# Kernel optimization log

Hardware: AMD Instinct MI355X
Metric: run time of the kernel (lower is better)

Reference implementation:

```python
import jax, jax.numpy as jnp
import numpy as np

INTERVAL = 0.02

def setup_inputs() -> dict:
    key = jax.random.key(0)
    ks = jax.random.split(key, 10)
    B, N, D, F = 8, 256, 64, 64
    return {
        "rbf_0": jax.random.normal(ks[0], (B, N, N, D), jnp.float32),
        "rbf_d": jax.random.normal(ks[1], (B, N, N, D), jnp.float32),
        "Q0_w": jax.random.normal(ks[2], (F, D), jnp.float32) * 0.1,
        "Q0_b": jax.random.normal(ks[3], (F,), jnp.float32) * 0.1,
        "Q_w": jax.random.normal(ks[4], (F, D), jnp.float32) * 0.1,
        "Q_b": jax.random.normal(ks[5], (F,), jnp.float32) * 0.1,
        "R0_w": jax.random.normal(ks[6], (F, D), jnp.float32) * 0.1,
        "R0_b": jax.random.normal(ks[7], (F,), jnp.float32) * 0.1,
        "R_w": jax.random.normal(ks[8], (F, D), jnp.float32) * 0.1,
        "R_b": jax.random.normal(ks[9], (F,), jnp.float32) * 0.1,
    }

def _linear(x, w, b):
    # x: [..., D], w: [F, D], b: [F] -> [..., F]
    return jnp.einsum('...d,fd->...f', x, w) + b

def reference(rbf_0, rbf_d, Q0_w, Q0_b, Q_w, Q_b, R0_w, R0_b, R_w, R_b):
    q_0 = _linear(rbf_0, Q0_w, Q0_b)   # [B, N, N, F]
    q = _linear(rbf_d, Q_w, Q_b)       # [B, N, N, F]
    r_0 = _linear(rbf_0, R0_w, R0_b)   # [B, N, N, F]
    r = _linear(rbf_d, R_w, R_b)       # [B, N, N, F]
    # 3-index correlator: contract over i and f
    C = jnp.einsum('bnif,bijf->bnj', q_0 * q, r_0 * r) * INTERVAL
    return C
```

## Files before the change

### kernel.cpp

```cpp
#include <hip/hip_runtime.h>
#include <hip/hip_bf16.h>


typedef __bf16 bf16x8 __attribute__((ext_vector_type(8)));
typedef float  f32x4  __attribute__((ext_vector_type(4)));
typedef int    i32x4  __attribute__((ext_vector_type(4)));

static __device__ __forceinline__ __bf16 f2bf(float x) {
  union { __hip_bfloat16 h; __bf16 b; } u;
  u.h = __float2bfloat16(x);
  return u.b;
}
static __device__ __forceinline__ unsigned short f2bfu(float x) {
  union { __hip_bfloat16 h; unsigned short s; } u;
  u.h = __float2bfloat16(x);
  return u.s;
}

__global__ __launch_bounds__(256, 1) void k_phase1(
    const float* __restrict__ rbf0, const float* __restrict__ rbfd,
    const float* __restrict__ Q0w, const float* __restrict__ Q0b,
    const float* __restrict__ Qw,  const float* __restrict__ Qb,
    const float* __restrict__ R0w, const float* __restrict__ R0b,
    const float* __restrict__ Rw,  const float* __restrict__ Rb,
    unsigned short* __restrict__ Aout, unsigned short* __restrict__ Bout)
{
  const int lane = threadIdx.x & 63;
  const int wave = threadIdx.x >> 6;
  const int fr   = lane & 15;
  const int kg   = lane >> 4;

  const float* Ws[4] = {Q0w, Qw, R0w, Rw};
  const float* Bs[4] = {Q0b, Qb, R0b, Rb};

  bf16x8 wf[4][2][4];
  float  bini[4][4];
#pragma unroll
  for (int m = 0; m < 4; ++m) {
#pragma unroll
    for (int kt = 0; kt < 2; ++kt)
#pragma unroll
      for (int ft = 0; ft < 4; ++ft) {
        const float* p = Ws[m] + (ft * 16 + fr) * 64 + kt * 32 + kg * 8;
        f32x4 lo = *(const f32x4*)p;
        f32x4 hi = *(const f32x4*)(p + 4);
        bf16x8 w;
#pragma unroll
        for (int j = 0; j < 4; ++j) { w[j] = f2bf(lo[j]); w[j + 4] = f2bf(hi[j]); }
        wf[m][kt][ft] = w;
      }
#pragma unroll
    for (int ft = 0; ft < 4; ++ft) bini[m][ft] = Bs[m][ft * 16 + fr];
  }

  const int stride = gridDim.x * 4;
  for (int t = blockIdx.x * 4 + wave; t < 32768; t += stride) {
    const float* x0 = rbf0 + (size_t)t * 1024 + fr * 64 + kg * 8;
    const float* xd = rbfd + (size_t)t * 1024 + fr * 64 + kg * 8;
    f32x4 q0 = *(const f32x4*)(x0);
    f32x4 q1 = *(const f32x4*)(x0 + 4);
    f32x4 q2 = *(const f32x4*)(x0 + 32);
    f32x4 q3 = *(const f32x4*)(x0 + 36);
    f32x4 e0 = *(const f32x4*)(xd);
    f32x4 e1 = *(const f32x4*)(xd + 4);
    f32x4 e2 = *(const f32x4*)(xd + 32);
    f32x4 e3 = *(const f32x4*)(xd + 36);

    bf16x8 a0[2], ad[2];
#pragma unroll
    for (int j = 0; j < 4; ++j) {
      a0[0][j] = f2bf(q0[j]); a0[0][j + 4] = f2bf(q1[j]);
      a0[1][j] = f2bf(q2[j]); a0[1][j + 4] = f2bf(q3[j]);
      ad[0][j] = f2bf(e0[j]); ad[0][j + 4] = f2bf(e1[j]);
      ad[1][j] = f2bf(e2[j]); ad[1][j + 4] = f2bf(e3[j]);
    }

    f32x4 acc[4][4];
#pragma unroll
    for (int m = 0; m < 4; ++m)
#pragma unroll
      for (int ft = 0; ft < 4; ++ft) {
        float bv = bini[m][ft];
        acc[m][ft][0] = bv; acc[m][ft][1] = bv; acc[m][ft][2] = bv; acc[m][ft][3] = bv;
      }

#pragma unroll
    for (int kt = 0; kt < 2; ++kt)
#pragma unroll
      for (int ft = 0; ft < 4; ++ft) {
        acc[0][ft] = __builtin_amdgcn_mfma_f32_16x16x32_bf16(a0[kt], wf[0][kt][ft], acc[0][ft], 0, 0, 0);
        acc[1][ft] = __builtin_amdgcn_mfma_f32_16x16x32_bf16(ad[kt], wf[1][kt][ft], acc[1][ft], 0, 0, 0);
        acc[2][ft] = __builtin_amdgcn_mfma_f32_16x16x32_bf16(a0[kt], wf[2][kt][ft], acc[2][ft], 0, 0, 0);
        acc[3][ft] = __builtin_amdgcn_mfma_f32_16x16x32_bf16(ad[kt], wf[3][kt][ft], acc[3][ft], 0, 0, 0);
      }

    const size_t base = (size_t)t * 1024;
#pragma unroll
    for (int ft = 0; ft < 4; ++ft)
#pragma unroll
      for (int r = 0; r < 4; ++r) {
        size_t off = base + (size_t)(kg * 4 + r) * 64 + ft * 16 + fr;
        Aout[off] = f2bfu(acc[0][ft][r] * acc[1][ft][r]);
        Bout[off] = f2bfu(acc[2][ft][r] * acc[3][ft][r]);
      }
  }
}

__global__ __launch_bounds__(256, 2) void k_phase2(
    const unsigned short* __restrict__ A, const unsigned short* __restrict__ Bm,
    float* __restrict__ C)
{
  __shared__ __align__(16) unsigned short Alds[128 * 64];
  __shared__ __align__(16) unsigned short Blds[128 * 64];

  const int tid  = threadIdx.x;
  const int lane = tid & 63;
  const int wave = tid >> 6;
  const int fr   = lane & 15;
  const int kg   = lane >> 4;

  const int bid = blockIdx.x;
  const int kc = bid & 7;
  const int jt = (bid >> 3) & 1;
  const int nt = (bid >> 4) & 1;
  const int b  = bid >> 5;
  const int n0 = nt * 128, j0 = jt * 128;
  const int wr = wave >> 1, wc = wave & 1;

  const unsigned short* Ab = A  + (size_t)b * 4194304;
  const unsigned short* Bb = Bm + (size_t)b * 4194304;

  f32x4 acc[4][4];
#pragma unroll
  for (int mt = 0; mt < 4; ++mt)
#pragma unroll
    for (int nn = 0; nn < 4; ++nn) {
      acc[mt][nn][0] = 0.f; acc[mt][nn][1] = 0.f; acc[mt][nn][2] = 0.f; acc[mt][nn][3] = 0.f;
    }

  for (int ii = 0; ii < 32; ++ii) {
    const int i = kc * 32 + ii;

    i32x4 va[4], vb[4];
#pragma unroll
    for (int rep = 0; rep < 4; ++rep) {
      int c = tid + rep * 256;
      int row = c >> 3, ch = c & 7;
      va[rep] = *(const i32x4*)(Ab + (size_t)(n0 + row) * 16384 + (size_t)i * 64 + ch * 8);
      vb[rep] = *(const i32x4*)(Bb + (size_t)i * 16384 + (size_t)(j0 + row) * 64 + ch * 8);
    }
    __syncthreads();
#pragma unroll
    for (int rep = 0; rep < 4; ++rep) {
      int c = tid + rep * 256;
      int row = c >> 3, ch = c & 7;
      int sw = ch ^ (row & 7);
      *(i32x4*)&Alds[row * 64 + sw * 8] = va[rep];
      *(i32x4*)&Blds[row * 64 + sw * 8] = vb[rep];
    }
    __syncthreads();

#pragma unroll
    for (int ks = 0; ks < 2; ++ks) {
      bf16x8 af[4], bfv[4];
#pragma unroll
      for (int mt = 0; mt < 4; ++mt) {
        int row = wr * 64 + mt * 16 + fr;
        int sw = (ks * 4 + kg) ^ (row & 7);
        af[mt] = *(const bf16x8*)&Alds[row * 64 + sw * 8];
      }
#pragma unroll
      for (int nn = 0; nn < 4; ++nn) {
        int row = wc * 64 + nn * 16 + fr;
        int sw = (ks * 4 + kg) ^ (row & 7);
        bfv[nn] = *(const bf16x8*)&Blds[row * 64 + sw * 8];
      }
#pragma unroll
      for (int mt = 0; mt < 4; ++mt)
#pragma unroll
        for (int nn = 0; nn < 4; ++nn)
          acc[mt][nn] = __builtin_amdgcn_mfma_f32_16x16x32_bf16(af[mt], bfv[nn], acc[mt][nn], 0, 0, 0);
    }
  }

  float* Cb = C + ((size_t)b << 16);
#pragma unroll
  for (int mt = 0; mt < 4; ++mt)
#pragma unroll
    for (int nn = 0; nn < 4; ++nn)
#pragma unroll
      for (int r = 0; r < 4; ++r) {
        int n = n0 + wr * 64 + mt * 16 + kg * 4 + r;
        int j = j0 + wc * 64 + nn * 16 + fr;
        atomicAdd(&Cb[n * 256 + j], acc[mt][nn][r] * 0.02f);
      }
}

extern "C" void kernel_launch(void* const* d_in, const int* in_sizes, int n_in,
                              void* d_out, int out_size, void* d_ws, size_t ws_size,
                              hipStream_t stream)
{
  const float* rbf0 = (const float*)d_in[0];
  const float* rbfd = (const float*)d_in[1];
  const float* Q0w  = (const float*)d_in[2];
  const float* Q0b  = (const float*)d_in[3];
  const float* Qw   = (const float*)d_in[4];
  const float* Qb   = (const float*)d_in[5];
  const float* R0w  = (const float*)d_in[6];
  const float* R0b  = (const float*)d_in[7];
  const float* Rw   = (const float*)d_in[8];
  const float* Rb   = (const float*)d_in[9];
  float* out = (float*)d_out;

  unsigned short* Abuf = (unsigned short*)d_ws;
  unsigned short* Bbuf = Abuf + (size_t)33554432;

  hipMemsetAsync(d_out, 0, (size_t)out_size * sizeof(float), stream);
  hipLaunchKernelGGL(k_phase1, dim3(512), dim3(256), 0, stream,
                     rbf0, rbfd, Q0w, Q0b, Qw, Qb, R0w, R0b, Rw, Rb, Abuf, Bbuf);
  hipLaunchKernelGGL(k_phase2, dim3(256), dim3(256), 0, stream, Abuf, Bbuf, out);
}
```

Measured before the change: 165.1 us.

## Split phase-1 waves by role, prefetch next tile, vectorize bf16 stores

Phase 1 now gives each wave pair one role, either the Q product or the R product. Each wave holds half as many weight fragments, which lowers register pressure, and the kernel allows higher occupancy (launch bounds 3, grid 1024). The MFMA operands are swapped so each lane holds 8 consecutive output features per row, turning 16 scalar 2-byte stores per array into two 16-byte vector stores. The next tile's input is software-prefetched into registers. In exchange, every rbf tile is now loaded twice, once by a Q wave and once by an R wave, which raises read traffic unless the cache absorbs it. Biases are rounded to bf16.

```diff
diff --git a/kernel.cpp b/kernel.cpp
--- a/kernel.cpp
+++ b/kernel.cpp
@@ -5,113 +5,151 @@
 typedef __bf16 bf16x8 __attribute__((ext_vector_type(8)));
 typedef float  f32x4  __attribute__((ext_vector_type(4)));
 typedef int    i32x4  __attribute__((ext_vector_type(4)));
+typedef unsigned short u16;
+typedef u16    u16x8  __attribute__((ext_vector_type(8)));
 
 static __device__ __forceinline__ __bf16 f2bf(float x) {
   union { __hip_bfloat16 h; __bf16 b; } u;
   u.h = __float2bfloat16(x);
   return u.b;
 }
-static __device__ __forceinline__ unsigned short f2bfu(float x) {
-  union { __hip_bfloat16 h; unsigned short s; } u;
+static __device__ __forceinline__ u16 f2bfu(float x) {
+  union { __hip_bfloat16 h; u16 s; } u;
   u.h = __float2bfloat16(x);
   return u.s;
 }
-
-__global__ __launch_bounds__(256, 1) void k_phase1(
+static __device__ __forceinline__ float bfu2f(u16 s) {
+  union { unsigned int u; float f; } v;
+  v.u = ((unsigned int)s) << 16;
+  return v.f;
+}
+
+__global__ __launch_bounds__(256, 3) void k_phase1(
     const float* __restrict__ rbf0, const float* __restrict__ rbfd,
     const float* __restrict__ Q0w, const float* __restrict__ Q0b,
     const float* __restrict__ Qw,  const float* __restrict__ Qb,
     const float* __restrict__ R0w, const float* __restrict__ R0b,
     const float* __restrict__ Rw,  const float* __restrict__ Rb,
-    unsigned short* __restrict__ Aout, unsigned short* __restrict__ Bout)
+    u16* __restrict__ Aout, u16* __restrict__ Bout)
 {
   const int lane = threadIdx.x & 63;
   const int wave = threadIdx.x >> 6;
   const int fr   = lane & 15;
   const int kg   = lane >> 4;
-
-  const float* Ws[4] = {Q0w, Qw, R0w, Rw};
-  const float* Bs[4] = {Q0b, Qb, R0b, Rb};
-
-  bf16x8 wf[4][2][4];
-  float  bini[4][4];
-#pragma unroll
-  for (int m = 0; m < 4; ++m) {
-#pragma unroll
-    for (int kt = 0; kt < 2; ++kt)
-#pragma unroll
-      for (int ft = 0; ft < 4; ++ft) {
-        const float* p = Ws[m] + (ft * 16 + fr) * 64 + kt * 32 + kg * 8;
-        f32x4 lo = *(const f32x4*)p;
-        f32x4 hi = *(const f32x4*)(p + 4);
-        bf16x8 w;
-#pragma unroll
-        for (int j = 0; j < 4; ++j) { w[j] = f2bf(lo[j]); w[j + 4] = f2bf(hi[j]); }
-        wf[m][kt][ft] = w;
-      }
-#pragma unroll
-    for (int ft = 0; ft < 4; ++ft) bini[m][ft] = Bs[m][ft * 16 + fr];
-  }
-
-  const int stride = gridDim.x * 4;
-  for (int t = blockIdx.x * 4 + wave; t < 32768; t += stride) {
+  const int role = wave >> 1;
+  const int sub  = wave & 1;
+
+  const float* W0 = role ? R0w : Q0w;
+  const float* W1 = role ? Rw  : Qw;
+  const float* B0 = role ? R0b : Q0b;
+  const float* B1 = role ? Rb  : Qb;
+  u16* __restrict__ Out = role ? Bout : Aout;
+
+  bf16x8 wf0[2][4], wf1[2][4];
+#pragma unroll
+  for (int kt = 0; kt < 2; ++kt)
+#pragma unroll
+    for (int ft = 0; ft < 4; ++ft) {
+      const float* p0 = W0 + (ft * 16 + fr) * 64 + kt * 32 + kg * 8;
+      const float* p1 = W1 + (ft * 16 + fr) * 64 + kt * 32 + kg * 8;
+      f32x4 a = *(const f32x4*)p0, b = *(const f32x4*)(p0 + 4);
+      f32x4 c = *(const f32x4*)p1, d = *(const f32x4*)(p1 + 4);
+      bf16x8 w0, w1;
+#pragma unroll
+      for (int j = 0; j < 4; ++j) {
+        w0[j] = f2bf(a[j]); w0[j + 4] = f2bf(b[j]);
+        w1[j] = f2bf(c[j]); w1[j + 4] = f2bf(d[j]);
+      }
+      wf0[kt][ft] = w0; wf1[kt][ft] = w1;
+    }
+
+  u16x8 pb0[2], pb1[2];
+#pragma unroll
+  for (int ft = 0; ft < 4; ++ft)
+#pragma unroll
+    for (int r = 0; r < 4; ++r) {
+      int idx = ft * 4 + r;
+      pb0[idx >> 3][idx & 7] = f2bfu(B0[ft * 16 + kg * 4 + r]);
+      pb1[idx >> 3][idx & 7] = f2bfu(B1[ft * 16 + kg * 4 + r]);
+    }
+
+  const int NT = 32768;
+  const int stride = gridDim.x * 2;
+  int t = blockIdx.x * 2 + sub;
+
+  f32x4 cur[8];
+  {
     const float* x0 = rbf0 + (size_t)t * 1024 + fr * 64 + kg * 8;
     const float* xd = rbfd + (size_t)t * 1024 + fr * 64 + kg * 8;
-    f32x4 q0 = *(const f32x4*)(x0);
-    f32x4 q1 = *(const f32x4*)(x0 + 4);
-    f32x4 q2 = *(const f32x4*)(x0 + 32);
-    f32x4 q3 = *(const f32x4*)(x0 + 36);
-    f32x4 e0 = *(const f32x4*)(xd);
-    f32x4 e1 = *(const f32x4*)(xd + 4);
-    f32x4 e2 = *(const f32x4*)(xd + 32);
-    f32x4 e3 = *(const f32x4*)(xd + 36);
-
-    bf16x8 a0[2], ad[2];
+    cur[0] = *(const f32x4*)(x0);      cur[1] = *(const f32x4*)(x0 + 4);
+    cur[2] = *(const f32x4*)(x0 + 32); cur[3] = *(const f32x4*)(x0 + 36);
+    cur[4] = *(const f32x4*)(xd);      cur[5] = *(const f32x4*)(xd + 4);
+    cur[6] = *(const f32x4*)(xd + 32); cur[7] = *(const f32x4*)(xd + 36);
+  }
+
+  while (t < NT) {
+    bf16x8 x0f[2], xdf[2];
 #pragma unroll
     for (int j = 0; j < 4; ++j) {
-      a0[0][j] = f2bf(q0[j]); a0[0][j + 4] = f2bf(q1[j]);
-      a0[1][j] = f2bf(q2[j]); a0[1][j + 4] = f2bf(q3[j]);
-      ad[0][j] = f2bf(e0[j]); ad[0][j + 4] = f2bf(e1[j]);
-      ad[1][j] = f2bf(e2[j]); ad[1][j + 4] = f2bf(e3[j]);
-    }
-
-    f32x4 acc[4][4];
-#pragma unroll
-    for (int m = 0; m < 4; ++m)
+      x0f[0][j] = f2bf(cur[0][j]); x0f[0][j + 4] = f2bf(cur[1][j]);
+      x0f[1][j] = f2bf(cur[2][j]); x0f[1][j + 4] = f2bf(cur[3][j]);
+      xdf[0][j] = f2bf(cur[4][j]); xdf[0][j + 4] = f2bf(cur[5][j]);
+      xdf[1][j] = f2bf(cur[6][j]); xdf[1][j + 4] = f2bf(cur[7][j]);
+    }
+
+    int tn = t + stride;
+    f32x4 nxt[8];
+    if (tn < NT) {
+      const float* x0 = rbf0 + (size_t)tn * 1024 + fr * 64 + kg * 8;
+      const float* xd = rbfd + (size_t)tn * 1024 + fr * 64 + kg * 8;
+      nxt[0] = *(const f32x4*)(x0);      nxt[1] = *(const f32x4*)(x0 + 4);
+      nxt[2] = *(const f32x4*)(x0 + 32); nxt[3] = *(const f32x4*)(x0 + 36);
+      nxt[4] = *(const f32x4*)(xd);      nxt[5] = *(const f32x4*)(xd + 4);
+      nxt[6] = *(const f32x4*)(xd + 32); nxt[7] = *(const f32x4*)(xd + 36);
+    }
+
+    f32x4 acc0[4], acc1[4];
+#pragma unroll
+    for (int ft = 0; ft < 4; ++ft)
+#pragma unroll
+      for (int r = 0; r < 4; ++r) {
+        int idx = ft * 4 + r;
+        acc0[ft][r] = bfu2f(pb0[idx >> 3][idx & 7]);
+        acc1[ft][r] = bfu2f(pb1[idx >> 3][idx & 7]);
+      }
+
+#pragma unroll
+    for (int kt = 0; kt < 2; ++kt)
 #pragma unroll
       for (int ft = 0; ft < 4; ++ft) {
-        float bv = bini[m][ft];
-        acc[m][ft][0] = bv; acc[m][ft][1] = bv; acc[m][ft][2] = bv; acc[m][ft][3] = bv;
-      }
-
-#pragma unroll
-    for (int kt = 0; kt < 2; ++kt)
-#pragma unroll
-      for (int ft = 0; ft < 4; ++ft) {
-        acc[0][ft] = __builtin_amdgcn_mfma_f32_16x16x32_bf16(a0[kt], wf[0][kt][ft], acc[0][ft], 0, 0, 0);
-        acc[1][ft] = __builtin_amdgcn_mfma_f32_16x16x32_bf16(ad[kt], wf[1][kt][ft], acc[1][ft], 0, 0, 0);
-        acc[2][ft] = __builtin_amdgcn_mfma_f32_16x16x32_bf16(a0[kt], wf[2][kt][ft], acc[2][ft], 0, 0, 0);
-        acc[3][ft] = __builtin_amdgcn_mfma_f32_16x16x32_bf16(ad[kt], wf[3][kt][ft], acc[3][ft], 0, 0, 0);
-      }
-
-    const size_t base = (size_t)t * 1024;
+        acc0[ft] = __builtin_amdgcn_mfma_f32_16x16x32_bf16(wf0[kt][ft], x0f[kt], acc0[ft], 0, 0, 0);
+        acc1[ft] = __builtin_amdgcn_mfma_f32_16x16x32_bf16(wf1[kt][ft], xdf[kt], acc1[ft], 0, 0, 0);
+      }
+
+    u16x8 o[2];
 #pragma unroll
     for (int ft = 0; ft < 4; ++ft)
 #pragma unroll
       for (int r = 0; r < 4; ++r) {
-        size_t off = base + (size_t)(kg * 4 + r) * 64 + ft * 16 + fr;
-        Aout[off] = f2bfu(acc[0][ft][r] * acc[1][ft][r]);
-        Bout[off] = f2bfu(acc[2][ft][r] * acc[3][ft][r]);
-      }
+        int idx = ft * 4 + r;
+        o[idx >> 3][idx & 7] = f2bfu(acc0[ft][r] * acc1[ft][r]);
+      }
+    u16* dst = Out + ((size_t)t * 16 + fr) * 64 + kg * 16;
+    *(u16x8*)dst       = o[0];
+    *(u16x8*)(dst + 8) = o[1];
+
+#pragma unroll
+    for (int i = 0; i < 8; ++i) cur[i] = nxt[i];
+    t = tn;
   }
 }
 
 __global__ __launch_bounds__(256, 2) void k_phase2(
-    const unsigned short* __restrict__ A, const unsigned short* __restrict__ Bm,
+    const u16* __restrict__ A, const u16* __restrict__ Bm,
     float* __restrict__ C)
 {
-  __shared__ __align__(16) unsigned short Alds[128 * 64];
-  __shared__ __align__(16) unsigned short Blds[128 * 64];
+  __shared__ __align__(16) u16 Alds[128 * 64];
+  __shared__ __align__(16) u16 Blds[128 * 64];
 
   const int tid  = threadIdx.x;
   const int lane = tid & 63;
@@ -127,8 +165,8 @@
   const int n0 = nt * 128, j0 = jt * 128;
   const int wr = wave >> 1, wc = wave & 1;
 
-  const unsigned short* Ab = A  + (size_t)b * 4194304;
-  const unsigned short* Bb = Bm + (size_t)b * 4194304;
+  const u16* Ab = A  + (size_t)b * 4194304;
+  const u16* Bb = Bm + (size_t)b * 4194304;
 
   f32x4 acc[4][4];
 #pragma unroll
@@ -212,11 +250,11 @@
   const float* Rb   = (const float*)d_in[9];
   float* out = (float*)d_out;
 
-  unsigned short* Abuf = (unsigned short*)d_ws;
-  unsigned short* Bbuf = Abuf + (size_t)33554432;
+  u16* Abuf = (u16*)d_ws;
+  u16* Bbuf = Abuf + (size_t)33554432;
 
   hipMemsetAsync(d_out, 0, (size_t)out_size * sizeof(float), stream);
-  hipLaunchKernelGGL(k_phase1, dim3(512), dim3(256), 0, stream,
+  hipLaunchKernelGGL(k_phase1, dim3(1024), dim3(256), 0, stream,
                      rbf0, rbfd, Q0w, Q0b, Qw, Qb, R0w, R0b, Rw, Rb, Abuf, Bbuf);
   hipLaunchKernelGGL(k_phase2, dim3(256), dim3(256), 0, stream, Abuf, Bbuf, out);
 }
```

Result: slower. 208.8 us (+26.4%).
